# Kernel tuning notes

Hardware: AMD Instinct MI355X
Metric: run time of the kernel (lower is better)

Reference implementation:

```python
import jax, jax.numpy as jnp
import numpy as np

N_HEADS = 16
EPS = 1e-12  # torch F.normalize eps


def setup_inputs() -> dict:
    key = jax.random.key(0)
    ks = jax.random.split(key, 10)
    bs, qlen, dim = 2, 2048, 1024
    s = 1.0 / np.sqrt(dim)
    inp = {
        "x": jax.random.normal(ks[0], (bs, qlen, dim), dtype=jnp.float32),
        "mask": jnp.ones((bs, qlen), dtype=jnp.int32),
        "Wq": jax.random.normal(ks[1], (dim, dim), dtype=jnp.float32) * s,
        "bq": jnp.zeros((dim,), dtype=jnp.float32),
        "Wk": jax.random.normal(ks[2], (dim, dim), dtype=jnp.float32) * s,
        "bk": jnp.zeros((dim,), dtype=jnp.float32),
        "Wv": jax.random.normal(ks[3], (dim, dim), dtype=jnp.float32) * s,
        "bv": jnp.zeros((dim,), dtype=jnp.float32),
        "Wo": jax.random.normal(ks[4], (dim, dim), dtype=jnp.float32) * s,
        "bo": jnp.zeros((dim,), dtype=jnp.float32),
        "scale": jnp.asarray(1.0 / np.sqrt(dim // N_HEADS), dtype=jnp.float32),
    }
    return inp


def reference(x, mask, Wq, bq, Wk, bk, Wv, bv, Wo, bo, scale):
    bs, qlen, dim = x.shape
    dph = dim // N_HEADS

    def shape_heads(t):  # [b, s, dim] -> [b, h, s, dph]
        return t.reshape(bs, -1, N_HEADS, dph).transpose(0, 2, 1, 3)

    q = shape_heads(x @ Wq + bq)
    k = shape_heads(x @ Wk + bk)
    v = shape_heads(x @ Wv + bv)

    # cosine attention: L2-normalize q, k; learned scalar scale
    q = q / jnp.maximum(jnp.linalg.norm(q, axis=-1, keepdims=True), EPS)
    k = k / jnp.maximum(jnp.linalg.norm(k, axis=-1, keepdims=True), EPS)
    q = q * scale

    scores = jnp.einsum("bhqd,bhkd->bhqk", q, k)  # [b,h,q,k]
    pad = (mask == 0)[:, None, None, :]  # [b,1,1,k]
    scores = jnp.where(pad, -jnp.inf, scores)
    weights = jax.nn.softmax(scores.astype(jnp.float32), axis=-1).astype(scores.dtype)
    ctx = jnp.einsum("bhqk,bhkd->bhqd", weights, v)
    ctx = ctx.transpose(0, 2, 1, 3).reshape(bs, qlen, dim)
    return ctx @ Wo + bo
```

## Files before the change

kernel.cpp:

```cpp
#include <hip/hip_runtime.h>
#include <math.h>

#define SEQ 2048
#define DIM 1024
#define NH 16
#define DPH 64
#define MTOT 4096

typedef __attribute__((ext_vector_type(8))) short bf16x8;
typedef __attribute__((ext_vector_type(4))) float f32x4;
typedef __attribute__((ext_vector_type(16))) float f32x16;
typedef __attribute__((ext_vector_type(4))) unsigned int u32x4;

__device__ __forceinline__ unsigned short f2bf(float f) {
    unsigned int u = __float_as_uint(f);
    return (unsigned short)((u + 0x7FFFu + ((u >> 16) & 1u)) >> 16);
}
__device__ __forceinline__ float bf2f(unsigned short h) {
    return __uint_as_float(((unsigned int)h) << 16);
}

__device__ __forceinline__ void stage16(const void* g, void* lds) {
    __builtin_amdgcn_global_load_lds((const __attribute__((address_space(1))) void*)g,
                                     (__attribute__((address_space(3))) void*)lds,
                                     16, 0, 0);
}

__device__ __forceinline__ unsigned cvtpk(float lo, float hi) {
    unsigned w;
    asm("v_cvt_pk_bf16_f32 %0, %1, %2" : "=v"(w) : "v"(lo), "v"(hi));
    return w;
}
__device__ __forceinline__ void plswap(unsigned &a, unsigned &b) {
    asm("v_permlane32_swap_b32 %0, %1" : "+v"(a), "+v"(b));
}

__global__ __launch_bounds__(256) void cast_x(const float* __restrict__ X,
                                              unsigned short* __restrict__ Xb)
{
    size_t i = (size_t)blockIdx.x * 256 + threadIdx.x;
    float4 v = *(const float4*)&X[i * 4];
    ushort4 o;
    o.x = f2bf(v.x); o.y = f2bf(v.y); o.z = f2bf(v.z); o.w = f2bf(v.w);
    *(ushort4*)&Xb[i * 4] = o;
}

__global__ __launch_bounds__(256) void prep_w(
    const float* __restrict__ Wq, const float* __restrict__ Wk,
    const float* __restrict__ Wv, const float* __restrict__ Wo,
    unsigned short* __restrict__ Wqt, unsigned short* __restrict__ Wkt,
    unsigned short* __restrict__ Wvt, unsigned short* __restrict__ Wot)
{
    const float* W; unsigned short* Wt;
    switch (blockIdx.z) {
        case 0: W = Wq; Wt = Wqt; break;
        case 1: W = Wk; Wt = Wkt; break;
        case 2: W = Wv; Wt = Wvt; break;
        default: W = Wo; Wt = Wot; break;
    }
    __shared__ float T[32][33];
    const int t = threadIdx.x;
    const int kt0 = blockIdx.y * 32;
    const int nt0 = blockIdx.x * 32;
    const int r = t >> 3, c4 = (t & 7) * 4;
    float4 v = *(const float4*)&W[(size_t)(kt0 + r) * DIM + nt0 + c4];
    T[r][c4 + 0] = v.x; T[r][c4 + 1] = v.y; T[r][c4 + 2] = v.z; T[r][c4 + 3] = v.w;
    __syncthreads();
    ushort4 o;
    o.x = f2bf(T[c4 + 0][r]);
    o.y = f2bf(T[c4 + 1][r]);
    o.z = f2bf(T[c4 + 2][r]);
    o.w = f2bf(T[c4 + 3][r]);
    *(ushort4*)&Wt[(size_t)(nt0 + r) * DIM + kt0 + c4] = o;
}

__global__ __launch_bounds__(256) void pack_mask(const int* __restrict__ mask,
                                                 unsigned long long* __restrict__ MB)
{
    const int w = blockIdx.x * 4 + (threadIdx.x >> 6);
    const int lane = threadIdx.x & 63;
    const int b = w >> 5, kt = w & 31;
    int m = mask[b * SEQ + kt * 64 + lane];
    unsigned long long bits = __ballot(m != 0);
    if (lane == 0) MB[w] = bits;
}

__device__ __forceinline__ void gemm_core(
    const unsigned short* __restrict__ Ab, const unsigned short* __restrict__ Bt,
    const float* __restrict__ bias, unsigned short* __restrict__ Cb,
    float* __restrict__ Cf, int mode)
{
    __shared__ __align__(16) unsigned short As[4096];
    __shared__ __align__(16) unsigned short Bs[4096];

    const int tid = threadIdx.x;
    const int l = tid & 63;
    const int w = tid >> 6;
    const int wm = w >> 1, wn = w & 1;
    const int lr = l & 15, lg = l >> 4;
    const int bm = blockIdx.y * 128;
    const int bn = blockIdx.x * 128;

    const unsigned short* a_src0 = Ab + (size_t)(bm + (2 * w) * 16 + lr) * DIM + lg * 8;
    const unsigned short* a_src1 = Ab + (size_t)(bm + (2 * w + 1) * 16 + lr) * DIM + lg * 8;
    const unsigned short* b_src0 = Bt + (size_t)(bn + (2 * w) * 16 + lr) * DIM + lg * 8;
    const unsigned short* b_src1 = Bt + (size_t)(bn + (2 * w + 1) * 16 + lr) * DIM + lg * 8;

    f32x4 acc[4][4];
#pragma unroll
    for (int i = 0; i < 4; ++i)
#pragma unroll
        for (int j = 0; j < 4; ++j) acc[i][j] = (f32x4){0.f, 0.f, 0.f, 0.f};

    for (int kk = 0; kk < DIM; kk += 32) {
        __syncthreads();
        stage16(a_src0 + kk, &As[(2 * w) * 512]);
        stage16(a_src1 + kk, &As[(2 * w + 1) * 512]);
        stage16(b_src0 + kk, &Bs[(2 * w) * 512]);
        stage16(b_src1 + kk, &Bs[(2 * w + 1) * 512]);
        __syncthreads();

        bf16x8 aF[4], bF[4];
#pragma unroll
        for (int i = 0; i < 4; ++i) {
            aF[i] = *(const bf16x8*)&As[(wm * 4 + i) * 512 + l * 8];
            bF[i] = *(const bf16x8*)&Bs[(wn * 4 + i) * 512 + l * 8];
        }
#pragma unroll
        for (int i = 0; i < 4; ++i)
#pragma unroll
            for (int j = 0; j < 4; ++j)
                acc[i][j] = __builtin_amdgcn_mfma_f32_16x16x32_bf16(aF[i], bF[j], acc[i][j], 0, 0, 0);
    }

#pragma unroll
    for (int i = 0; i < 4; ++i) {
#pragma unroll
        for (int j = 0; j < 4; ++j) {
            const int n = bn + wn * 64 + j * 16 + lr;
            const float bv = bias[n];
            const int m0 = bm + wm * 64 + i * 16 + lg * 4;
            if (mode == 0) {
#pragma unroll
                for (int p = 0; p < 4; ++p)
                    Cb[(size_t)(m0 + p) * DIM + n] = f2bf(acc[i][j][p] + bv);
            } else if (mode == 1) {
                const int b = m0 >> 11, s = m0 & 2047;
                const int h = n >> 6, d = n & 63;
                ushort4 o;
                o.x = f2bf(acc[i][j][0] + bv);
                o.y = f2bf(acc[i][j][1] + bv);
                o.z = f2bf(acc[i][j][2] + bv);
                o.w = f2bf(acc[i][j][3] + bv);
                *(ushort4*)&Cb[((size_t)((b * NH + h) * DPH + d)) * SEQ + s] = o;
            } else {
#pragma unroll
                for (int p = 0; p < 4; ++p)
                    Cf[(size_t)(m0 + p) * DIM + n] = acc[i][j][p] + bv;
            }
        }
    }
}

__global__ __launch_bounds__(256) void qkv_gemm(
    const unsigned short* __restrict__ Xb,
    const unsigned short* __restrict__ Wqt, const unsigned short* __restrict__ Wkt,
    const unsigned short* __restrict__ Wvt,
    const float* __restrict__ bq, const float* __restrict__ bk, const float* __restrict__ bv,
    unsigned short* __restrict__ Qb, unsigned short* __restrict__ Kb,
    unsigned short* __restrict__ Vtb)
{
    if (blockIdx.z == 0)      gemm_core(Xb, Wqt, bq, Qb,  nullptr, 0);
    else if (blockIdx.z == 1) gemm_core(Xb, Wkt, bk, Kb,  nullptr, 0);
    else                      gemm_core(Xb, Wvt, bv, Vtb, nullptr, 1);
}

__global__ __launch_bounds__(256) void o_gemm(
    const unsigned short* __restrict__ Ab, const unsigned short* __restrict__ Wot,
    const float* __restrict__ bo, float* __restrict__ Out)
{
    gemm_core(Ab, Wot, bo, nullptr, Out, 2);
}

__global__ __launch_bounds__(256) void norm_qk(
    unsigned short* __restrict__ Qb, unsigned short* __restrict__ Kb,
    const float* __restrict__ scale_p)
{
    const int row = blockIdx.x;
    const int tid = threadIdx.x;
    unsigned short* buf = (tid < 128) ? Qb : Kb;
    const int g = tid & 127;
    const size_t base = (size_t)row * DIM + g * 8;
    ushort4 v0 = *(ushort4*)&buf[base];
    ushort4 v1 = *(ushort4*)&buf[base + 4];
    float f[8] = {bf2f(v0.x), bf2f(v0.y), bf2f(v0.z), bf2f(v0.w),
                  bf2f(v1.x), bf2f(v1.y), bf2f(v1.z), bf2f(v1.w)};
    float s = 0.f;
#pragma unroll
    for (int i = 0; i < 8; ++i) s = fmaf(f[i], f[i], s);
    s += __shfl_xor(s, 1);
    s += __shfl_xor(s, 2);
    s += __shfl_xor(s, 4);
    const float scl = ((tid < 128) ? (*scale_p * 1.44269504088896340736f) : 1.0f)
                      / fmaxf(sqrtf(s), 1e-12f);
    ushort4 o0, o1;
    o0.x = f2bf(f[0] * scl); o0.y = f2bf(f[1] * scl);
    o0.z = f2bf(f[2] * scl); o0.w = f2bf(f[3] * scl);
    o1.x = f2bf(f[4] * scl); o1.y = f2bf(f[5] * scl);
    o1.z = f2bf(f[6] * scl); o1.w = f2bf(f[7] * scl);
    *(ushort4*)&buf[base] = o0;
    *(ushort4*)&buf[base + 4] = o1;
}

__global__ __launch_bounds__(256) void attn(
    const unsigned short* __restrict__ Qb, const unsigned short* __restrict__ Kb,
    const unsigned short* __restrict__ Vtb, const unsigned long long* __restrict__ MB,
    unsigned short* __restrict__ CTXb)
{
    __shared__ __align__(16) unsigned short Ks[2][4096];
    __shared__ __align__(16) unsigned short Vts[2][4096];

    const int tid = threadIdx.x;
    const int l = tid & 63;
    const int w = tid >> 6;
    const int l31 = l & 31;
    const int hi = l >> 5;
    const int qt = blockIdx.x, h = blockIdx.y, b = blockIdx.z;

    const size_t qrow = (size_t)(b * SEQ + qt * 128 + w * 32 + l31);
    bf16x8 qf[4];
#pragma unroll
    for (int df = 0; df < 4; ++df)
        qf[df] = *(const bf16x8*)&Qb[qrow * DIM + h * DPH + df * 16 + hi * 8];

    const int sub = l >> 3, ss = (l & 7) ^ sub;
    const unsigned short* Kptr  = Kb  + (size_t)(b * SEQ) * DIM + h * DPH;
    const unsigned short* Vtptr = Vtb + ((size_t)(b * NH + h) * DPH) * SEQ;
    const unsigned long long* mbp = MB + b * 32;

    f32x16 ctx0 = {}, ctx1 = {};
    float lsum = 0.f;

    {
        const int r0 = w * 16, r1 = w * 16 + 8;
        stage16(Kptr + (size_t)(r0 + sub) * DIM + ss * 8, &Ks[0][r0 * 64]);
        stage16(Kptr + (size_t)(r1 + sub) * DIM + ss * 8, &Ks[0][r1 * 64]);
        stage16(Vtptr + (size_t)(r0 + sub) * SEQ + ss * 8, &Vts[0][r0 * 64]);
        stage16(Vtptr + (size_t)(r1 + sub) * SEQ + ss * 8, &Vts[0][r1 * 64]);
    }

    for (int kt = 0; kt < SEQ / 64; ++kt) {
        __syncthreads();
        const int cur = kt & 1;
        if (kt + 1 < SEQ / 64) {
            const int nxt = cur ^ 1;
            const int r0 = w * 16, r1 = w * 16 + 8;
            const size_t ko = (size_t)((kt + 1) * 64);
            stage16(Kptr + (ko + r0 + sub) * DIM + ss * 8, &Ks[nxt][r0 * 64]);
            stage16(Kptr + (ko + r1 + sub) * DIM + ss * 8, &Ks[nxt][r1 * 64]);
            stage16(Vtptr + (size_t)(r0 + sub) * SEQ + ko + ss * 8, &Vts[nxt][r0 * 64]);
            stage16(Vtptr + (size_t)(r1 + sub) * SEQ + ko + ss * 8, &Vts[nxt][r1 * 64]);
        }

        const char* kbase = (const char*)Ks[cur];
        f32x16 S0 = {}, S1 = {};
#pragma unroll
        for (int df = 0; df < 4; ++df) {
            const int so = ((df * 2 + hi) ^ (l31 & 7)) << 4;
            bf16x8 k0 = *(const bf16x8*)(kbase + l31 * 128 + so);
            bf16x8 k1 = *(const bf16x8*)(kbase + (32 + l31) * 128 + so);
            S0 = __builtin_amdgcn_mfma_f32_32x32x16_bf16(k0, qf[df], S0, 0, 0, 0);
            S1 = __builtin_amdgcn_mfma_f32_32x32x16_bf16(k1, qf[df], S1, 0, 0, 0);
        }

        float p[32];
#pragma unroll
        for (int r = 0; r < 16; ++r) {
            p[r]      = __builtin_amdgcn_exp2f(S0[r]);
            p[16 + r] = __builtin_amdgcn_exp2f(S1[r]);
        }

        const unsigned long long bits = mbp[kt];
        if (bits != ~0ull) {
#pragma unroll
            for (int r = 0; r < 16; ++r) {
                const int key0 = (r & 3) + 8 * (r >> 2) + 4 * hi;
                p[r]      *= (float)((bits >> key0) & 1);
                p[16 + r] *= (float)((bits >> (32 + key0)) & 1);
            }
        }

#pragma unroll
        for (int r = 0; r < 32; ++r) lsum += p[r];

        bf16x8 pa[4];
#pragma unroll
        for (int krow = 0; krow < 2; ++krow) {
            const float* pp = &p[krow * 16];
            unsigned w01[4], w23[4];
#pragma unroll
            for (int a = 0; a < 4; ++a) {
                w01[a] = cvtpk(pp[4 * a + 0], pp[4 * a + 1]);
                w23[a] = cvtpk(pp[4 * a + 2], pp[4 * a + 3]);
            }
#pragma unroll
            for (int fh = 0; fh < 2; ++fh) {
                unsigned A0 = w01[2 * fh], B0 = w01[2 * fh + 1];
                unsigned A1 = w23[2 * fh], B1 = w23[2 * fh + 1];
                plswap(A0, B0);
                plswap(A1, B1);
                u32x4 t = {A0, A1, B0, B1};
                union { u32x4 u; bf16x8 v; } cvt;
                cvt.u = t;
                pa[krow * 2 + fh] = cvt.v;
            }
        }

        const char* vbase = (const char*)Vts[cur];
#pragma unroll
        for (int kf2 = 0; kf2 < 4; ++kf2) {
            const int so = ((kf2 * 2 + hi) ^ (l31 & 7)) << 4;
            bf16x8 v0 = *(const bf16x8*)(vbase + l31 * 128 + so);
            bf16x8 v1 = *(const bf16x8*)(vbase + (32 + l31) * 128 + so);
            ctx0 = __builtin_amdgcn_mfma_f32_32x32x16_bf16(pa[kf2], v0, ctx0, 0, 0, 0);
            ctx1 = __builtin_amdgcn_mfma_f32_32x32x16_bf16(pa[kf2], v1, ctx1, 0, 0, 0);
        }
    }

    lsum += __shfl_xor(lsum, 32);
    const float inv = 1.0f / lsum;

    const size_t orow0 = (size_t)(b * SEQ + qt * 128 + w * 32);
#pragma unroll
    for (int r = 0; r < 16; ++r) {
        const int q = (r & 3) + 8 * (r >> 2) + 4 * hi;
        const float invr = __shfl(inv, q);
        const size_t ro = (orow0 + q) * DIM + h * DPH;
        CTXb[ro + l31]      = f2bf(ctx0[r] * invr);
        CTXb[ro + 32 + l31] = f2bf(ctx1[r] * invr);
    }
}

extern "C" void kernel_launch(void* const* d_in, const int* in_sizes, int n_in,
                              void* d_out, int out_size, void* d_ws, size_t ws_size,
                              hipStream_t stream)
{
    const float* x    = (const float*)d_in[0];
    const int*   mask = (const int*)d_in[1];
    const float* Wq   = (const float*)d_in[2];
    const float* bq   = (const float*)d_in[3];
    const float* Wk   = (const float*)d_in[4];
    const float* bk   = (const float*)d_in[5];
    const float* Wv   = (const float*)d_in[6];
    const float* bv   = (const float*)d_in[7];
    const float* Wo   = (const float*)d_in[8];
    const float* bo   = (const float*)d_in[9];
    const float* scale = (const float*)d_in[10];
    float* out = (float*)d_out;

    char* p = (char*)d_ws;
    unsigned short* Xb  = (unsigned short*)p; p += (size_t)MTOT * DIM * 2;
    unsigned short* Wqt = (unsigned short*)p; p += (size_t)DIM * DIM * 2;
    unsigned short* Wkt = (unsigned short*)p; p += (size_t)DIM * DIM * 2;
    unsigned short* Wvt = (unsigned short*)p; p += (size_t)DIM * DIM * 2;
    unsigned short* Wot = (unsigned short*)p; p += (size_t)DIM * DIM * 2;
    unsigned short* Qb  = (unsigned short*)p; p += (size_t)MTOT * DIM * 2;
    unsigned short* Kb  = (unsigned short*)p; p += (size_t)MTOT * DIM * 2;
    unsigned short* Vtb = (unsigned short*)p; p += (size_t)MTOT * DIM * 2;
    unsigned short* CTXb = (unsigned short*)p; p += (size_t)MTOT * DIM * 2;
    unsigned long long* MBits = (unsigned long long*)p;

    cast_x<<<dim3(MTOT * DIM / 4 / 256), 256, 0, stream>>>(x, Xb);
    prep_w<<<dim3(32, 32, 4), 256, 0, stream>>>(Wq, Wk, Wv, Wo, Wqt, Wkt, Wvt, Wot);
    pack_mask<<<dim3(16), 256, 0, stream>>>(mask, MBits);
    qkv_gemm<<<dim3(DIM / 128, MTOT / 128, 3), 256, 0, stream>>>(
        Xb, Wqt, Wkt, Wvt, bq, bk, bv, Qb, Kb, Vtb);
    norm_qk<<<dim3(MTOT), 256, 0, stream>>>(Qb, Kb, scale);
    attn<<<dim3(SEQ / 128, NH, 2), 256, 0, stream>>>(Qb, Kb, Vtb, MBits, CTXb);
    o_gemm<<<dim3(DIM / 128, MTOT / 128, 1), 256, 0, stream>>>(CTXb, Wot, bo, out);
}
```

Before: 254.9 us.

## Fuse QK L2-normalization into GEMM epilogue, double-buffer GEMM LDS, remap blocks across XCDs

The separate norm_qk kernel is removed. The Q/K projection GEMM epilogue now computes per-head row norms with lane shuffles across the 64-column wave tile and writes normalized, scaled bf16 directly. The GEMM mainloop gains double-buffered LDS staging, so the next k-tile's loads are issued before the current tile's MFMAs, with one barrier per iteration. Block indices in the GEMMs and attention are remapped so neighbouring tiles land on the same XCD for L2 reuse. Together these remove a full read-write pass over Q and K and an extra launch, at the cost of doubled LDS use.

```diff
diff --git a/kernel.cpp b/kernel.cpp
--- a/kernel.cpp
+++ b/kernel.cpp
@@ -33,6 +33,20 @@
 }
 __device__ __forceinline__ void plswap(unsigned &a, unsigned &b) {
     asm("v_permlane32_swap_b32 %0, %1" : "+v"(a), "+v"(b));
+}
+
+__device__ __forceinline__ void xcd_remap(int gx, int gy, int gz,
+                                          int &x, int &y, int &z)
+{
+    const int h = (blockIdx.z * gy + blockIdx.y) * gx + blockIdx.x;
+    const int nb = gx * gy * gz;
+    const int chunk = nb >> 3;
+    const int l = (h & 7) * chunk + (h >> 3);
+    const int P = gx * gz;
+    y = l / P;
+    const int r = l - y * P;
+    z = r / gx;
+    x = r - z * gx;
 }
 
 __global__ __launch_bounds__(256) void cast_x(const float* __restrict__ X,
@@ -88,18 +102,18 @@
 __device__ __forceinline__ void gemm_core(
     const unsigned short* __restrict__ Ab, const unsigned short* __restrict__ Bt,
     const float* __restrict__ bias, unsigned short* __restrict__ Cb,
-    float* __restrict__ Cf, int mode)
-{
-    __shared__ __align__(16) unsigned short As[4096];
-    __shared__ __align__(16) unsigned short Bs[4096];
+    float* __restrict__ Cf, int mode, int bx, int by, float qs)
+{
+    __shared__ __align__(16) unsigned short As[2][4096];
+    __shared__ __align__(16) unsigned short Bs[2][4096];
 
     const int tid = threadIdx.x;
     const int l = tid & 63;
     const int w = tid >> 6;
     const int wm = w >> 1, wn = w & 1;
     const int lr = l & 15, lg = l >> 4;
-    const int bm = blockIdx.y * 128;
-    const int bn = blockIdx.x * 128;
+    const int bm = by * 128;
+    const int bn = bx * 128;
 
     const unsigned short* a_src0 = Ab + (size_t)(bm + (2 * w) * 16 + lr) * DIM + lg * 8;
     const unsigned short* a_src1 = Ab + (size_t)(bm + (2 * w + 1) * 16 + lr) * DIM + lg * 8;
@@ -112,51 +126,96 @@
 #pragma unroll
         for (int j = 0; j < 4; ++j) acc[i][j] = (f32x4){0.f, 0.f, 0.f, 0.f};
 
+    stage16(a_src0, &As[0][(2 * w) * 512]);
+    stage16(a_src1, &As[0][(2 * w + 1) * 512]);
+    stage16(b_src0, &Bs[0][(2 * w) * 512]);
+    stage16(b_src1, &Bs[0][(2 * w + 1) * 512]);
+
+    int t = 0;
     for (int kk = 0; kk < DIM; kk += 32) {
         __syncthreads();
-        stage16(a_src0 + kk, &As[(2 * w) * 512]);
-        stage16(a_src1 + kk, &As[(2 * w + 1) * 512]);
-        stage16(b_src0 + kk, &Bs[(2 * w) * 512]);
-        stage16(b_src1 + kk, &Bs[(2 * w + 1) * 512]);
-        __syncthreads();
-
+        if (kk + 32 < DIM) {
+            const int nxt = t ^ 1;
+            stage16(a_src0 + kk + 32, &As[nxt][(2 * w) * 512]);
+            stage16(a_src1 + kk + 32, &As[nxt][(2 * w + 1) * 512]);
+            stage16(b_src0 + kk + 32, &Bs[nxt][(2 * w) * 512]);
+            stage16(b_src1 + kk + 32, &Bs[nxt][(2 * w + 1) * 512]);
+        }
         bf16x8 aF[4], bF[4];
 #pragma unroll
         for (int i = 0; i < 4; ++i) {
-            aF[i] = *(const bf16x8*)&As[(wm * 4 + i) * 512 + l * 8];
-            bF[i] = *(const bf16x8*)&Bs[(wn * 4 + i) * 512 + l * 8];
+            aF[i] = *(const bf16x8*)&As[t][(wm * 4 + i) * 512 + l * 8];
+            bF[i] = *(const bf16x8*)&Bs[t][(wn * 4 + i) * 512 + l * 8];
         }
 #pragma unroll
         for (int i = 0; i < 4; ++i)
 #pragma unroll
             for (int j = 0; j < 4; ++j)
                 acc[i][j] = __builtin_amdgcn_mfma_f32_16x16x32_bf16(aF[i], bF[j], acc[i][j], 0, 0, 0);
-    }
-
-#pragma unroll
-    for (int i = 0; i < 4; ++i) {
-#pragma unroll
-        for (int j = 0; j < 4; ++j) {
-            const int n = bn + wn * 64 + j * 16 + lr;
-            const float bv = bias[n];
+        t ^= 1;
+    }
+
+    float bvj[4];
+#pragma unroll
+    for (int j = 0; j < 4; ++j) bvj[j] = bias[bn + wn * 64 + j * 16 + lr];
+#pragma unroll
+    for (int i = 0; i < 4; ++i)
+#pragma unroll
+        for (int j = 0; j < 4; ++j)
+#pragma unroll
+            for (int p = 0; p < 4; ++p) acc[i][j][p] += bvj[j];
+
+    if (mode == 0) {
+#pragma unroll
+        for (int i = 0; i < 4; ++i) {
+            float scl[4];
+#pragma unroll
+            for (int p = 0; p < 4; ++p) {
+                float s = 0.f;
+#pragma unroll
+                for (int j = 0; j < 4; ++j) s = fmaf(acc[i][j][p], acc[i][j][p], s);
+                s += __shfl_xor(s, 1);
+                s += __shfl_xor(s, 2);
+                s += __shfl_xor(s, 4);
+                s += __shfl_xor(s, 8);
+                scl[p] = qs / fmaxf(sqrtf(s), 1e-12f);
+            }
             const int m0 = bm + wm * 64 + i * 16 + lg * 4;
-            if (mode == 0) {
+#pragma unroll
+            for (int j = 0; j < 4; ++j) {
+                const int n = bn + wn * 64 + j * 16 + lr;
 #pragma unroll
                 for (int p = 0; p < 4; ++p)
-                    Cb[(size_t)(m0 + p) * DIM + n] = f2bf(acc[i][j][p] + bv);
-            } else if (mode == 1) {
-                const int b = m0 >> 11, s = m0 & 2047;
+                    Cb[(size_t)(m0 + p) * DIM + n] = f2bf(acc[i][j][p] * scl[p]);
+            }
+        }
+    } else if (mode == 1) {
+#pragma unroll
+        for (int i = 0; i < 4; ++i) {
+            const int m0 = bm + wm * 64 + i * 16 + lg * 4;
+            const int b = m0 >> 11, s = m0 & 2047;
+#pragma unroll
+            for (int j = 0; j < 4; ++j) {
+                const int n = bn + wn * 64 + j * 16 + lr;
                 const int h = n >> 6, d = n & 63;
                 ushort4 o;
-                o.x = f2bf(acc[i][j][0] + bv);
-                o.y = f2bf(acc[i][j][1] + bv);
-                o.z = f2bf(acc[i][j][2] + bv);
-                o.w = f2bf(acc[i][j][3] + bv);
+                o.x = f2bf(acc[i][j][0]);
+                o.y = f2bf(acc[i][j][1]);
+                o.z = f2bf(acc[i][j][2]);
+                o.w = f2bf(acc[i][j][3]);
                 *(ushort4*)&Cb[((size_t)((b * NH + h) * DPH + d)) * SEQ + s] = o;
-            } else {
+            }
+        }
+    } else {
+#pragma unroll
+        for (int i = 0; i < 4; ++i) {
+            const int m0 = bm + wm * 64 + i * 16 + lg * 4;
+#pragma unroll
+            for (int j = 0; j < 4; ++j) {
+                const int n = bn + wn * 64 + j * 16 + lr;
 #pragma unroll
                 for (int p = 0; p < 4; ++p)
-                    Cf[(size_t)(m0 + p) * DIM + n] = acc[i][j][p] + bv;
+                    Cf[(size_t)(m0 + p) * DIM + n] = acc[i][j][p];
             }
         }
     }
@@ -167,49 +226,27 @@
     const unsigned short* __restrict__ Wqt, const unsigned short* __restrict__ Wkt,
     const unsigned short* __restrict__ Wvt,
     const float* __restrict__ bq, const float* __restrict__ bk, const float* __restrict__ bv,
+    const float* __restrict__ scale_p,
     unsigned short* __restrict__ Qb, unsigned short* __restrict__ Kb,
     unsigned short* __restrict__ Vtb)
 {
-    if (blockIdx.z == 0)      gemm_core(Xb, Wqt, bq, Qb,  nullptr, 0);
-    else if (blockIdx.z == 1) gemm_core(Xb, Wkt, bk, Kb,  nullptr, 0);
-    else                      gemm_core(Xb, Wvt, bv, Vtb, nullptr, 1);
+    int x, y, z;
+    xcd_remap(8, 32, 3, x, y, z);
+    if (z == 0)
+        gemm_core(Xb, Wqt, bq, Qb, nullptr, 0, x, y, scale_p[0] * 1.44269504088896340736f);
+    else if (z == 1)
+        gemm_core(Xb, Wkt, bk, Kb, nullptr, 0, x, y, 1.0f);
+    else
+        gemm_core(Xb, Wvt, bv, Vtb, nullptr, 1, x, y, 1.0f);
 }
 
 __global__ __launch_bounds__(256) void o_gemm(
     const unsigned short* __restrict__ Ab, const unsigned short* __restrict__ Wot,
     const float* __restrict__ bo, float* __restrict__ Out)
 {
-    gemm_core(Ab, Wot, bo, nullptr, Out, 2);
-}
-
-__global__ __launch_bounds__(256) void norm_qk(
-    unsigned short* __restrict__ Qb, unsigned short* __restrict__ Kb,
-    const float* __restrict__ scale_p)
-{
-    const int row = blockIdx.x;
-    const int tid = threadIdx.x;
-    unsigned short* buf = (tid < 128) ? Qb : Kb;
-    const int g = tid & 127;
-    const size_t base = (size_t)row * DIM + g * 8;
-    ushort4 v0 = *(ushort4*)&buf[base];
-    ushort4 v1 = *(ushort4*)&buf[base + 4];
-    float f[8] = {bf2f(v0.x), bf2f(v0.y), bf2f(v0.z), bf2f(v0.w),
-                  bf2f(v1.x), bf2f(v1.y), bf2f(v1.z), bf2f(v1.w)};
-    float s = 0.f;
-#pragma unroll
-    for (int i = 0; i < 8; ++i) s = fmaf(f[i], f[i], s);
-    s += __shfl_xor(s, 1);
-    s += __shfl_xor(s, 2);
-    s += __shfl_xor(s, 4);
-    const float scl = ((tid < 128) ? (*scale_p * 1.44269504088896340736f) : 1.0f)
-                      / fmaxf(sqrtf(s), 1e-12f);
-    ushort4 o0, o1;
-    o0.x = f2bf(f[0] * scl); o0.y = f2bf(f[1] * scl);
-    o0.z = f2bf(f[2] * scl); o0.w = f2bf(f[3] * scl);
-    o1.x = f2bf(f[4] * scl); o1.y = f2bf(f[5] * scl);
-    o1.z = f2bf(f[6] * scl); o1.w = f2bf(f[7] * scl);
-    *(ushort4*)&buf[base] = o0;
-    *(ushort4*)&buf[base + 4] = o1;
+    int x, y, z;
+    xcd_remap(8, 32, 1, x, y, z);
+    gemm_core(Ab, Wot, bo, nullptr, Out, 2, x, y, 1.0f);
 }
 
 __global__ __launch_bounds__(256) void attn(
@@ -225,7 +262,16 @@
     const int w = tid >> 6;
     const int l31 = l & 31;
     const int hi = l >> 5;
-    const int qt = blockIdx.x, h = blockIdx.y, b = blockIdx.z;
+
+    int qt, h, b;
+    {
+        const int hh = (blockIdx.z * 16 + blockIdx.y) * 16 + blockIdx.x;
+        const int ll = (hh & 7) * 64 + (hh >> 3);
+        qt = ll & 15;
+        const int g = ll >> 4;
+        h = g & 15;
+        b = g >> 4;
+    }
 
     const size_t qrow = (size_t)(b * SEQ + qt * 128 + w * 32 + l31);
     bf16x8 qf[4];
@@ -309,9 +355,9 @@
                 unsigned A1 = w23[2 * fh], B1 = w23[2 * fh + 1];
                 plswap(A0, B0);
                 plswap(A1, B1);
-                u32x4 t = {A0, A1, B0, B1};
+                u32x4 tt = {A0, A1, B0, B1};
                 union { u32x4 u; bf16x8 v; } cvt;
-                cvt.u = t;
+                cvt.u = tt;
                 pa[krow * 2 + fh] = cvt.v;
             }
         }
@@ -373,9 +419,8 @@
     cast_x<<<dim3(MTOT * DIM / 4 / 256), 256, 0, stream>>>(x, Xb);
     prep_w<<<dim3(32, 32, 4), 256, 0, stream>>>(Wq, Wk, Wv, Wo, Wqt, Wkt, Wvt, Wot);
     pack_mask<<<dim3(16), 256, 0, stream>>>(mask, MBits);
-    qkv_gemm<<<dim3(DIM / 128, MTOT / 128, 3), 256, 0, stream>>>(
-        Xb, Wqt, Wkt, Wvt, bq, bk, bv, Qb, Kb, Vtb);
-    norm_qk<<<dim3(MTOT), 256, 0, stream>>>(Qb, Kb, scale);
-    attn<<<dim3(SEQ / 128, NH, 2), 256, 0, stream>>>(Qb, Kb, Vtb, MBits, CTXb);
-    o_gemm<<<dim3(DIM / 128, MTOT / 128, 1), 256, 0, stream>>>(CTXb, Wot, bo, out);
-}
+    qkv_gemm<<<dim3(8, 32, 3), 256, 0, stream>>>(
+        Xb, Wqt, Wkt, Wvt, bq, bk, bv, scale, Qb, Kb, Vtb);
+    attn<<<dim3(16, 16, 2), 256, 0, stream>>>(Qb, Kb, Vtb, MBits, CTXb);
+    o_gemm<<<dim3(8, 32, 1), 256, 0, stream>>>(CTXb, Wot, bo, out);
+}
```

After: 239.6 us. -6.0%, faster.
